# Kernel optimization log

Hardware: AMD Instinct MI355X
Metric: run time of the kernel (lower is better)

## Reference

```python
import jax, jax.numpy as jnp
import numpy as np

N, B, HID, NPG, DEG, N_HOPS = 102400, 512, 256, 200, 32, 2
E = N * DEG
LN_EPS = 1e-5


def setup_inputs() -> dict:
    key = jax.random.key(0)
    ks = jax.random.split(key, 8)
    h = jax.random.normal(ks[0], (N, HID), jnp.float32)
    g = jax.random.normal(ks[1], (B, HID), jnp.float32)
    # sorted node->graph assignment, 200 nodes per graph
    batch = jnp.repeat(jnp.arange(B, dtype=jnp.int32), NPG)
    # intra-graph random edges: graph id per edge + local endpoints
    gid = jax.random.randint(ks[2], (E,), 0, B, jnp.int32)
    s_loc = jax.random.randint(ks[3], (E,), 0, NPG, jnp.int32)
    d_loc = jax.random.randint(ks[4], (E,), 0, NPG, jnp.int32)
    edge_index = jnp.stack([gid * NPG + s_loc, gid * NPG + d_loc])  # [2, E]
    # head MLP params: Linear(HID,2HID) -> LayerNorm(2HID) -> ReLU -> Linear(2HID,1)
    W1 = jax.random.normal(ks[5], (HID, 2 * HID), jnp.float32) * (1.0 / np.sqrt(HID))
    b1 = jnp.zeros((2 * HID,), jnp.float32)
    ln_g = jnp.ones((2 * HID,), jnp.float32)
    ln_b = jnp.zeros((2 * HID,), jnp.float32)
    W2 = jax.random.normal(ks[6], (2 * HID, 1), jnp.float32) * (1.0 / np.sqrt(2 * HID))
    b2 = jnp.zeros((1,), jnp.float32)
    return {"h": h, "g": g, "batch": batch, "edge_index": edge_index,
            "W1": W1, "b1": b1, "ln_g": ln_g, "ln_b": ln_b, "W2": W2, "b2": b2}


def reference(h, g, batch, edge_index, W1, b1, ln_g, ln_b, W2, b2):
    n = h.shape[0]
    nb = g.shape[0]
    # repeat_interleave(g, bincount(batch)) == g[batch] for sorted batch
    x = h + g[batch]                                   # [N, HID]
    z = x @ W1 + b1                                    # [N, 2*HID]
    mu = jnp.mean(z, axis=-1, keepdims=True)
    var = jnp.var(z, axis=-1, keepdims=True)           # biased, as torch LayerNorm
    z = (z - mu) * jax.lax.rsqrt(var + LN_EPS) * ln_g + ln_b
    z = jax.nn.relu(z)
    logits = (z @ W2 + b2)[:, 0]                       # [N]
    # segment softmax over each graph
    m = jax.ops.segment_max(logits, batch, num_segments=nb)
    e = jnp.exp(logits - m[batch])
    s = jax.ops.segment_sum(e, batch, num_segments=nb)
    node_prob = e / s[batch]                           # [N]
    pmax = jax.ops.segment_max(node_prob, batch, num_segments=nb)
    cand = jnp.where(node_prob >= pmax[batch], jnp.arange(n, dtype=jnp.int32), n)
    seed = jax.ops.segment_min(cand, batch, num_segments=nb)   # [B] global node ids
    # k_hop_subgraph BFS (PyG flow='source_to_target': expand target -> source)
    src, dst = edge_index[0], edge_index[1]
    nm = jnp.zeros((n,), jnp.int32).at[seed].set(1)
    for _ in range(N_HOPS):
        nm = jnp.maximum(nm, jnp.zeros((n,), jnp.int32).at[src].max(nm[dst]))
    nmb = nm > 0
    edge_mask = nmb[src] & nmb[dst]                    # [E] kept-edge mask
    edge_weight = logits[src] + logits[dst]            # [E]
    em = edge_mask.astype(jnp.int32)
    node_mask = (jnp.zeros((n,), jnp.int32).at[src].max(em).at[dst].max(em)) > 0
    return node_prob, edge_weight, edge_mask, node_mask
```

## Files before the change

kernel.cpp:

```cpp
#include <hip/hip_runtime.h>
#include <hip/hip_bf16.h>

#define HID 256
#define HID2 512
#define NPG 200
#define LN_EPS 1e-5f

typedef float f32x4 __attribute__((ext_vector_type(4)));
typedef short s16x8 __attribute__((ext_vector_type(8)));
typedef unsigned short ushort_t;

__device__ __forceinline__ ushort_t f2bf_rne(float x) {
    union { float f; unsigned int u; } c; c.f = x;
    unsigned int u = c.u;
    return (ushort_t)((u + 0x7fffu + ((u >> 16) & 1u)) >> 16);
}
__device__ __forceinline__ float bf2f(ushort_t h) {
    union { unsigned int u; float f; } c; c.u = ((unsigned int)h) << 16;
    return c.f;
}

__global__ __launch_bounds__(256)
void w1_prep_kernel(const float* __restrict__ W1,
                    ushort_t* __restrict__ w1h, ushort_t* __restrict__ w1l)
{
    const int col = blockIdx.x;
    const int k   = threadIdx.x;
    const float v = W1[(size_t)k * HID2 + col];
    const ushort_t hi = f2bf_rne(v);
    const ushort_t lo = f2bf_rne(v - bf2f(hi));
    const int tile = col >> 4, lc = col & 15;
    const int kq = k >> 5, gq = (k >> 3) & 3, j = k & 7;
    const size_t idx = ((((size_t)tile << 3) + kq) * 64 + (gq << 4) + lc) * 8 + j;
    w1h[idx] = hi;
    w1l[idx] = lo;
}

__global__ __launch_bounds__(512, 4)
void mlp_logits_mfma(const float* __restrict__ h, const float* __restrict__ g,
                     const int* __restrict__ batch,
                     const ushort_t* __restrict__ w1h, const ushort_t* __restrict__ w1l,
                     const float* __restrict__ b1,
                     const float* __restrict__ lng, const float* __restrict__ lnb,
                     const float* __restrict__ W2, const float* __restrict__ b2,
                     float* __restrict__ logits)
{
    __shared__ ushort_t xsh[64 * 256];
    __shared__ ushort_t xsl[64 * 256];
    __shared__ float prm[4 * 512];
    __shared__ float redS1[8][64];
    __shared__ float redS2[8][64];
    __shared__ float redT[8][64];
    __shared__ float muv[64], rsv[64];

    const int tid  = threadIdx.x;
    const int row0 = blockIdx.x * 64;

    {
        const int c = tid;
        prm[c]        = b1[c];
        prm[512 + c]  = lng[c];
        prm[1024 + c] = lnb[c];
        prm[1536 + c] = W2[c];
    }

    #pragma unroll
    for (int i = 0; i < 4; ++i) {
        const int ci = tid + (i << 9);
        const int r  = ci >> 5;
        const int kc = (ci & 31) << 3;
        const int grow = row0 + r;
        const int gb   = batch[grow];
        const float4* hp = reinterpret_cast<const float4*>(h + (size_t)grow * HID + kc);
        const float4* gp = reinterpret_cast<const float4*>(g + (size_t)gb   * HID + kc);
        const float4 h0 = hp[0], h1 = hp[1];
        const float4 g0 = gp[0], g1 = gp[1];
        float xv[8] = { h0.x + g0.x, h0.y + g0.y, h0.z + g0.z, h0.w + g0.w,
                        h1.x + g1.x, h1.y + g1.y, h1.z + g1.z, h1.w + g1.w };
        ushort_t hh[8], ll[8];
        #pragma unroll
        for (int j = 0; j < 8; ++j) {
            const ushort_t hi = f2bf_rne(xv[j]);
            hh[j] = hi;
            ll[j] = f2bf_rne(xv[j] - bf2f(hi));
        }
        int byte_off = r * 512 + (kc << 1);
        byte_off ^= (r & 7) << 4;
        *reinterpret_cast<s16x8*>(reinterpret_cast<char*>(xsh) + byte_off) =
            *reinterpret_cast<const s16x8*>(hh);
        *reinterpret_cast<s16x8*>(reinterpret_cast<char*>(xsl) + byte_off) =
            *reinterpret_cast<const s16x8*>(ll);
    }
    __syncthreads();

    const int w  = tid >> 6;
    const int l  = tid & 63;
    const int lc = l & 15;
    const int gq = l >> 4;
    const int wcol0 = w << 6;

    f32x4 acc[4][4];
    #pragma unroll
    for (int rt = 0; rt < 4; ++rt)
        #pragma unroll
        for (int ct = 0; ct < 4; ++ct) acc[rt][ct] = (f32x4){0.f, 0.f, 0.f, 0.f};

    const ushort_t* bfh = w1h + (((size_t)w << 2) << 3) * 512 + (size_t)l * 8;
    const ushort_t* bfl = w1l + (((size_t)w << 2) << 3) * 512 + (size_t)l * 8;

    for (int kq = 0; kq < 8; ++kq) {
        s16x8 bh[4], bl[4];
        #pragma unroll
        for (int ct = 0; ct < 4; ++ct) {
            const size_t foff = (size_t)((ct << 3) + kq) * 512;
            bh[ct] = *reinterpret_cast<const s16x8*>(bfh + foff);
            bl[ct] = *reinterpret_cast<const s16x8*>(bfl + foff);
        }
        s16x8 ah[4], al[4];
        #pragma unroll
        for (int rt = 0; rt < 4; ++rt) {
            const int arow = (rt << 4) | lc;
            int abyte = arow * 512 + (((kq << 5) + (gq << 3)) << 1);
            abyte ^= (arow & 7) << 4;
            ah[rt] = *reinterpret_cast<const s16x8*>(
                         reinterpret_cast<const char*>(xsh) + abyte);
            al[rt] = *reinterpret_cast<const s16x8*>(
                         reinterpret_cast<const char*>(xsl) + abyte);
        }
        #pragma unroll
        for (int ct = 0; ct < 4; ++ct)
            #pragma unroll
            for (int rt = 0; rt < 4; ++rt)
                acc[rt][ct] = __builtin_amdgcn_mfma_f32_16x16x32_bf16(ah[rt], bh[ct], acc[rt][ct], 0, 0, 0);
        #pragma unroll
        for (int ct = 0; ct < 4; ++ct)
            #pragma unroll
            for (int rt = 0; rt < 4; ++rt)
                acc[rt][ct] = __builtin_amdgcn_mfma_f32_16x16x32_bf16(al[rt], bh[ct], acc[rt][ct], 0, 0, 0);
        #pragma unroll
        for (int ct = 0; ct < 4; ++ct)
            #pragma unroll
            for (int rt = 0; rt < 4; ++rt)
                acc[rt][ct] = __builtin_amdgcn_mfma_f32_16x16x32_bf16(ah[rt], bl[ct], acc[rt][ct], 0, 0, 0);
    }

    #pragma unroll
    for (int rt = 0; rt < 4; ++rt) {
        float s1[4] = {0.f, 0.f, 0.f, 0.f};
        float s2[4] = {0.f, 0.f, 0.f, 0.f};
        #pragma unroll
        for (int ct = 0; ct < 4; ++ct) {
            const float bb = prm[wcol0 + (ct << 4) + lc];
            #pragma unroll
            for (int reg = 0; reg < 4; ++reg) {
                const float v = acc[rt][ct][reg] + bb;
                acc[rt][ct][reg] = v;
                s1[reg] += v;
                s2[reg] = fmaf(v, v, s2[reg]);
            }
        }
        #pragma unroll
        for (int reg = 0; reg < 4; ++reg) {
            float a = s1[reg], q = s2[reg];
            a += __shfl_xor(a, 1); q += __shfl_xor(q, 1);
            a += __shfl_xor(a, 2); q += __shfl_xor(q, 2);
            a += __shfl_xor(a, 4); q += __shfl_xor(q, 4);
            a += __shfl_xor(a, 8); q += __shfl_xor(q, 8);
            if (lc == 0) {
                const int row = (rt << 4) + (gq << 2) + reg;
                redS1[w][row] = a;
                redS2[w][row] = q;
            }
        }
    }
    __syncthreads();

    if (tid < 64) {
        float S1 = 0.f, S2 = 0.f;
        #pragma unroll
        for (int i = 0; i < 8; ++i) { S1 += redS1[i][tid]; S2 += redS2[i][tid]; }
        const float mu = S1 * (1.0f / HID2);
        const float var = S2 * (1.0f / HID2) - mu * mu;
        muv[tid] = mu;
        rsv[tid] = rsqrtf(var + LN_EPS);
    }
    __syncthreads();

    #pragma unroll
    for (int rt = 0; rt < 4; ++rt) {
        float tpart[4] = {0.f, 0.f, 0.f, 0.f};
        float mus[4], rss[4];
        #pragma unroll
        for (int reg = 0; reg < 4; ++reg) {
            const int row = (rt << 4) + (gq << 2) + reg;
            mus[reg] = muv[row];
            rss[reg] = rsv[row];
        }
        #pragma unroll
        for (int ct = 0; ct < 4; ++ct) {
            const int c = wcol0 + (ct << 4) + lc;
            const float lg = prm[512 + c], lb = prm[1024 + c], w2 = prm[1536 + c];
            #pragma unroll
            for (int reg = 0; reg < 4; ++reg) {
                float zn = (acc[rt][ct][reg] - mus[reg]) * rss[reg] * lg + lb;
                zn = fmaxf(zn, 0.f);
                tpart[reg] = fmaf(zn, w2, tpart[reg]);
            }
        }
        #pragma unroll
        for (int reg = 0; reg < 4; ++reg) {
            float t = tpart[reg];
            t += __shfl_xor(t, 1); t += __shfl_xor(t, 2);
            t += __shfl_xor(t, 4); t += __shfl_xor(t, 8);
            if (lc == 0) redT[w][(rt << 4) + (gq << 2) + reg] = t;
        }
    }
    __syncthreads();

    if (tid < 64) {
        float t = 0.f;
        #pragma unroll
        for (int i = 0; i < 8; ++i) t += redT[i][tid];
        logits[row0 + tid] = t + b2[0];
    }
}

__global__ __launch_bounds__(256)
void softmax_seed_kernel(const float* __restrict__ logits,
                         float* __restrict__ out_prob,
                         unsigned char* __restrict__ nm)
{
    const int gid  = blockIdx.x;
    const int tid  = threadIdx.x;
    const int node = gid * NPG + tid;
    const bool act = tid < NPG;

    __shared__ float redf[4];
    __shared__ int   redi[4];

    float l = act ? logits[node] : -INFINITY;

    float m = l;
    #pragma unroll
    for (int off = 32; off >= 1; off >>= 1) m = fmaxf(m, __shfl_xor(m, off));
    if ((tid & 63) == 0) redf[tid >> 6] = m;
    __syncthreads();
    const float bm = fmaxf(fmaxf(redf[0], redf[1]), fmaxf(redf[2], redf[3]));
    __syncthreads();

    const float e = act ? expf(l - bm) : 0.0f;
    float s = e;
    #pragma unroll
    for (int off = 32; off >= 1; off >>= 1) s += __shfl_xor(s, off);
    if ((tid & 63) == 0) redf[tid >> 6] = s;
    __syncthreads();
    const float bs = redf[0] + redf[1] + redf[2] + redf[3];
    __syncthreads();

    const float p = act ? e / bs : -1.0f;
    if (act) out_prob[node] = p;

    float pm = p;
    #pragma unroll
    for (int off = 32; off >= 1; off >>= 1) pm = fmaxf(pm, __shfl_xor(pm, off));
    if ((tid & 63) == 0) redf[tid >> 6] = pm;
    __syncthreads();
    const float bpm = fmaxf(fmaxf(redf[0], redf[1]), fmaxf(redf[2], redf[3]));

    int c = (act && p >= bpm) ? node : 0x7FFFFFFF;
    #pragma unroll
    for (int off = 32; off >= 1; off >>= 1) c = min(c, __shfl_xor(c, off));
    if ((tid & 63) == 0) redi[tid >> 6] = c;
    __syncthreads();
    if (tid == 0) {
        const int seed = min(min(redi[0], redi[1]), min(redi[2], redi[3]));
        nm[seed] = 1;
    }
}

__global__ __launch_bounds__(256)
void bfs_pass_kernel(const int* __restrict__ ei, unsigned char* __restrict__ nm,
                     const int E, const int maxlvl, const int newlvl)
{
    const int stride = gridDim.x * blockDim.x;
    for (int e = blockIdx.x * blockDim.x + threadIdx.x; e < E; e += stride) {
        const int d  = ei[E + e];
        const int lv = nm[d];
        if (lv >= 1 && lv <= maxlvl) {
            const int s = ei[e];
            if (nm[s] == 0) nm[s] = (unsigned char)newlvl;
        }
    }
}

__global__ __launch_bounds__(256)
void edge_out_kernel(const int* __restrict__ ei, const float* __restrict__ logits,
                     const unsigned char* __restrict__ nm,
                     float* __restrict__ out_ew,
                     float* __restrict__ out_em,
                     unsigned char* __restrict__ nodemask, const int E)
{
    const int stride = gridDim.x * blockDim.x;
    for (int e = blockIdx.x * blockDim.x + threadIdx.x; e < E; e += stride) {
        const int s = ei[e];
        const int d = ei[E + e];
        const float lw = logits[s] + logits[d];
        const bool em  = (nm[s] != 0) && (nm[d] != 0);
        out_ew[e] = lw;
        out_em[e] = em ? 1.0f : 0.0f;
        if (em) { nodemask[s] = 1; nodemask[d] = 1; }
    }
}

__global__ __launch_bounds__(256)
void node_mask_kernel(const unsigned char* __restrict__ nodemask,
                      float* __restrict__ out_nm, const int N)
{
    const int stride = gridDim.x * blockDim.x;
    for (int i = blockIdx.x * blockDim.x + threadIdx.x; i < N; i += stride)
        out_nm[i] = nodemask[i] ? 1.0f : 0.0f;
}

__global__ __launch_bounds__(256)
void zero_ws_kernel(uint4* __restrict__ p, const int n16)
{
    const int i = blockIdx.x * blockDim.x + threadIdx.x;
    if (i < n16) p[i] = make_uint4(0u, 0u, 0u, 0u);
}

extern "C" void kernel_launch(void* const* d_in, const int* in_sizes, int n_in,
                              void* d_out, int out_size, void* d_ws, size_t ws_size,
                              hipStream_t stream)
{
    const float* h     = (const float*)d_in[0];
    const float* g     = (const float*)d_in[1];
    const int*   batch = (const int*)d_in[2];
    const int*   ei    = (const int*)d_in[3];
    const float* W1    = (const float*)d_in[4];
    const float* b1    = (const float*)d_in[5];
    const float* lng   = (const float*)d_in[6];
    const float* lnb   = (const float*)d_in[7];
    const float* W2    = (const float*)d_in[8];
    const float* b2    = (const float*)d_in[9];

    const int N = in_sizes[2];
    const int E = in_sizes[3] / 2;

    float* out        = (float*)d_out;
    float* out_prob   = out;
    float* out_ew     = out + N;
    float* out_em     = out + (size_t)N + E;
    float* out_nmask  = out + (size_t)N + 2 * (size_t)E;

    char* ws = (char*)d_ws;
    float*         logits   = (float*)ws;
    ushort_t*      w1h      = (ushort_t*)(ws + (size_t)N * 4);
    ushort_t*      w1l      = (ushort_t*)(ws + (size_t)N * 4 + 262144);
    unsigned char* nm       = (unsigned char*)(ws + (size_t)N * 4 + 524288);
    unsigned char* nodemask = nm + N;

    const int n16 = (2 * N) / 16;
    zero_ws_kernel<<<(n16 + 255) / 256, 256, 0, stream>>>((uint4*)nm, n16);

    w1_prep_kernel<<<HID2, HID, 0, stream>>>(W1, w1h, w1l);

    mlp_logits_mfma<<<N / 64, 512, 0, stream>>>(h, g, batch, w1h, w1l,
                                                b1, lng, lnb, W2, b2, logits);
    softmax_seed_kernel<<<N / NPG, 256, 0, stream>>>(logits, out_prob, nm);
    bfs_pass_kernel<<<4096, 256, 0, stream>>>(ei, nm, E, 1, 2);
    bfs_pass_kernel<<<4096, 256, 0, stream>>>(ei, nm, E, 2, 3);
    edge_out_kernel<<<4096, 256, 0, stream>>>(ei, logits, nm, out_ew, out_em,
                                              nodemask, E);
    node_mask_kernel<<<512, 256, 0, stream>>>(nodemask, out_nmask, N);
}
```

Before: 233.1 us.

## Split bf16x3 GEMM into three passes with register double-buffered B fragments

Restructures the split-bf16 GEMM loop into three separate K-passes (hi*hi, lo*hi, hi*lo). Each pass prefetches the next K-step's W1 fragments into registers while the current MFMAs run, which should hide global-load latency and lower peak register pressure. The h activation reads also become nontemporal loads so streamed data does not pollute cache. In exchange, the A fragments in LDS and the B fragments are each read more times, and the loop structure adds extra iterations.

```diff
diff --git a/kernel.cpp b/kernel.cpp
--- a/kernel.cpp
+++ b/kernel.cpp
@@ -71,10 +71,11 @@
         const int kc = (ci & 31) << 3;
         const int grow = row0 + r;
         const int gb   = batch[grow];
-        const float4* hp = reinterpret_cast<const float4*>(h + (size_t)grow * HID + kc);
-        const float4* gp = reinterpret_cast<const float4*>(g + (size_t)gb   * HID + kc);
-        const float4 h0 = hp[0], h1 = hp[1];
-        const float4 g0 = gp[0], g1 = gp[1];
+        const f32x4* hp = reinterpret_cast<const f32x4*>(h + (size_t)grow * HID + kc);
+        const f32x4* gp = reinterpret_cast<const f32x4*>(g + (size_t)gb   * HID + kc);
+        const f32x4 h0 = __builtin_nontemporal_load(hp);
+        const f32x4 h1 = __builtin_nontemporal_load(hp + 1);
+        const f32x4 g0 = gp[0], g1 = gp[1];
         float xv[8] = { h0.x + g0.x, h0.y + g0.y, h0.z + g0.z, h0.w + g0.w,
                         h1.x + g1.x, h1.y + g1.y, h1.z + g1.z, h1.w + g1.w };
         ushort_t hh[8], ll[8];
@@ -108,41 +109,41 @@
     const ushort_t* bfh = w1h + (((size_t)w << 2) << 3) * 512 + (size_t)l * 8;
     const ushort_t* bfl = w1l + (((size_t)w << 2) << 3) * 512 + (size_t)l * 8;
 
-    for (int kq = 0; kq < 8; ++kq) {
-        s16x8 bh[4], bl[4];
-        #pragma unroll
-        for (int ct = 0; ct < 4; ++ct) {
-            const size_t foff = (size_t)((ct << 3) + kq) * 512;
-            bh[ct] = *reinterpret_cast<const s16x8*>(bfh + foff);
-            bl[ct] = *reinterpret_cast<const s16x8*>(bfl + foff);
-        }
-        s16x8 ah[4], al[4];
-        #pragma unroll
-        for (int rt = 0; rt < 4; ++rt) {
-            const int arow = (rt << 4) | lc;
-            int abyte = arow * 512 + (((kq << 5) + (gq << 3)) << 1);
-            abyte ^= (arow & 7) << 4;
-            ah[rt] = *reinterpret_cast<const s16x8*>(
-                         reinterpret_cast<const char*>(xsh) + abyte);
-            al[rt] = *reinterpret_cast<const s16x8*>(
-                         reinterpret_cast<const char*>(xsl) + abyte);
-        }
+    auto gemm_pass = [&](const ushort_t* asrc, const ushort_t* bb) {
+        const char* ab = reinterpret_cast<const char*>(asrc);
+        s16x8 bcur[4], bnxt[4];
         #pragma unroll
         for (int ct = 0; ct < 4; ++ct)
-            #pragma unroll
-            for (int rt = 0; rt < 4; ++rt)
-                acc[rt][ct] = __builtin_amdgcn_mfma_f32_16x16x32_bf16(ah[rt], bh[ct], acc[rt][ct], 0, 0, 0);
-        #pragma unroll
-        for (int ct = 0; ct < 4; ++ct)
-            #pragma unroll
-            for (int rt = 0; rt < 4; ++rt)
-                acc[rt][ct] = __builtin_amdgcn_mfma_f32_16x16x32_bf16(al[rt], bh[ct], acc[rt][ct], 0, 0, 0);
-        #pragma unroll
-        for (int ct = 0; ct < 4; ++ct)
-            #pragma unroll
-            for (int rt = 0; rt < 4; ++rt)
-                acc[rt][ct] = __builtin_amdgcn_mfma_f32_16x16x32_bf16(ah[rt], bl[ct], acc[rt][ct], 0, 0, 0);
-    }
+            bcur[ct] = *reinterpret_cast<const s16x8*>(bb + (size_t)(ct << 3) * 512);
+        for (int kq = 0; kq < 8; ++kq) {
+            if (kq < 7) {
+                #pragma unroll
+                for (int ct = 0; ct < 4; ++ct)
+                    bnxt[ct] = *reinterpret_cast<const s16x8*>(
+                                   bb + (size_t)((ct << 3) + kq + 1) * 512);
+            }
+            s16x8 af[4];
+            #pragma unroll
+            for (int rt = 0; rt < 4; ++rt) {
+                const int arow = (rt << 4) | lc;
+                int abyte = arow * 512 + (((kq << 5) + (gq << 3)) << 1);
+                abyte ^= (arow & 7) << 4;
+                af[rt] = *reinterpret_cast<const s16x8*>(ab + abyte);
+            }
+            #pragma unroll
+            for (int ct = 0; ct < 4; ++ct)
+                #pragma unroll
+                for (int rt = 0; rt < 4; ++rt)
+                    acc[rt][ct] = __builtin_amdgcn_mfma_f32_16x16x32_bf16(
+                                      af[rt], bcur[ct], acc[rt][ct], 0, 0, 0);
+            #pragma unroll
+            for (int ct = 0; ct < 4; ++ct) bcur[ct] = bnxt[ct];
+        }
+    };
+
+    gemm_pass(xsh, bfh);
+    gemm_pass(xsl, bfh);
+    gemm_pass(xsh, bfl);
 
     #pragma unroll
     for (int rt = 0; rt < 4; ++rt) {
```

New measurement: 713.8 us. 206% more time.
